# Kernel optimization log

Hardware: AMD Instinct MI355X
Metric: run time of the kernel (lower is better)

## Reference

```python
import jax, jax.numpy as jnp
import numpy as np
import math

DIM = 1024
THETA = 10000.0


def rope_cos_sin(seq_len, dim, dtype=jnp.float32):
    # freqs over pairs: 1/theta^(2i/dim), angles = t * freq
    inv = 1.0 / (THETA ** (jnp.arange(0, dim, 2, dtype=jnp.float32) / dim))  # [dim/2]
    t = jnp.arange(seq_len, dtype=jnp.float32)
    ang = jnp.outer(t, inv)  # [S, dim/2]
    return jnp.cos(ang).astype(dtype), jnp.sin(ang).astype(dtype)


def apply_rotary(x, cos, sin):
    # x: [B, S, D]; treat consecutive pairs as complex (xr + i*xi)
    B, S, D = x.shape
    xr = x[..., 0::2]  # [B, S, D/2]
    xi = x[..., 1::2]
    or_ = xr * cos - xi * sin
    oi_ = xr * sin + xi * cos
    # interleave back: (..., D/2, 2) -> (..., D)
    return jnp.stack([or_, oi_], axis=-1).reshape(B, S, D)


def setup_inputs() -> dict:
    key = jax.random.key(0)
    ks = jax.random.split(key, 5)
    B, S, D = 4, 2048, DIM
    x = jax.random.normal(ks[0], (B, S, D), dtype=jnp.float32)
    s = 1.0 / math.sqrt(D)
    wq = jax.random.normal(ks[1], (D, D), dtype=jnp.float32) * s
    wk = jax.random.normal(ks[2], (D, D), dtype=jnp.float32) * s
    wv = jax.random.normal(ks[3], (D, D), dtype=jnp.float32) * s
    wo = jax.random.normal(ks[4], (D, D), dtype=jnp.float32) * s
    return {"x": x, "wq": wq, "wk": wk, "wv": wv, "wo": wo}


def reference(x, wq, wk, wv, wo):
    B, S, D = x.shape
    xq = jnp.einsum('bsd,ed->bse', x, wq)  # Linear: x @ W^T
    xk = jnp.einsum('bsd,ed->bse', x, wk)
    xv = jnp.einsum('bsd,ed->bse', x, wv)
    cos, sin = rope_cos_sin(S, D, x.dtype)
    xq = apply_rotary(xq, cos, sin)
    xk = apply_rotary(xk, cos, sin)
    scores = jnp.einsum('bqd,bkd->bqk', xq, xk) / jnp.sqrt(jnp.asarray(D, x.dtype))
    attn = jax.nn.softmax(scores, axis=-1)  # no causal mask in original
    out = jnp.einsum('bqk,bkd->bqd', attn, xv)
    return jnp.einsum('bsd,ed->bse', out, wo)
```

## Files before the change

kernel.cpp:

```cpp
#include <hip/hip_runtime.h>
#include <math.h>

typedef __attribute__((ext_vector_type(8))) short short8;
typedef __attribute__((ext_vector_type(4))) float f32x4;
typedef unsigned short u16;

__device__ __forceinline__ float b2f(u16 u) {
    union { unsigned u; float f; } c; c.u = ((unsigned)u) << 16; return c.f;
}
__device__ __forceinline__ u16 f2b(float f) {
    unsigned u = __float_as_uint(f);
    u += 0x7fffu + ((u >> 16) & 1u);
    return (u16)(u >> 16);
}

__device__ __forceinline__ void gl_lds16(const u16* g, u16* l) {
    __builtin_amdgcn_global_load_lds(
        (const __attribute__((address_space(1))) void*)g,
        (__attribute__((address_space(3))) void*)l,
        16, 0, 0);
}

__global__ __launch_bounds__(256) void cvt_f32_bf16(const float* __restrict__ src,
                                                    u16* __restrict__ dst, int n) {
    const int i = (blockIdx.x * 256 + threadIdx.x) * 8;
    if (i >= n) return;
    const float4 a = *(const float4*)&src[i];
    const float4 b = *(const float4*)&src[i + 4];
    short8 o;
    o[0] = (short)f2b(a.x); o[1] = (short)f2b(a.y);
    o[2] = (short)f2b(a.z); o[3] = (short)f2b(a.w);
    o[4] = (short)f2b(b.x); o[5] = (short)f2b(b.y);
    o[6] = (short)f2b(b.z); o[7] = (short)f2b(b.w);
    *(short8*)&dst[i] = o;
}

__global__ __launch_bounds__(256) void cvt_weights(
    const float* __restrict__ w0, const float* __restrict__ w1,
    const float* __restrict__ w2, const float* __restrict__ w3,
    u16* __restrict__ dst) {
    const int z = blockIdx.z;
    const float* src = (z == 0) ? w0 : (z == 1) ? w1 : (z == 2) ? w2 : w3;
    const int i = (blockIdx.x * 256 + threadIdx.x) * 8;
    const float4 a = *(const float4*)&src[i];
    const float4 b = *(const float4*)&src[i + 4];
    short8 o;
    o[0] = (short)f2b(a.x); o[1] = (short)f2b(a.y);
    o[2] = (short)f2b(a.z); o[3] = (short)f2b(a.w);
    o[4] = (short)f2b(b.x); o[5] = (short)f2b(b.y);
    o[6] = (short)f2b(b.z); o[7] = (short)f2b(b.w);
    *(short8*)&dst[(long)z * 1024 * 1024 + i] = o;
}

template<typename OT>
__device__ __forceinline__ void gemm_body(
    const u16* __restrict__ A, const u16* __restrict__ W, OT* __restrict__ C,
    int lda, int ldw, int ldc, int K, float scale, int tm, int tn)
{
    __shared__ u16 lsA[2][128 * 32];
    __shared__ u16 lsB[2][128 * 32];

    const int m0 = tm * 128;
    const int n0 = tn * 128;
    const int t = threadIdx.x;
    const int lane = t & 63;
    const int wave = t >> 6;
    const int wm = (wave & 1) * 64;
    const int wn = (wave >> 1) * 64;

    const int sr = t >> 2;
    const int scol = ((t & 3) ^ ((t >> 3) & 3)) * 8;

    const int offA0 = (m0 + sr) * lda + scol;
    const int offA1 = offA0 + 64 * lda;
    const int offW0 = (n0 + sr) * ldw + scol;
    const int offW1 = offW0 + 64 * ldw;
    const u16* Au = A;
    const u16* Wu = W;

    f32x4 acc[4][4];
#pragma unroll
    for (int i = 0; i < 4; ++i)
#pragma unroll
        for (int j = 0; j < 4; ++j)
            acc[i][j] = (f32x4){0.f, 0.f, 0.f, 0.f};

    const int fr = lane & 15;
    const int fq = lane >> 4;
    const int swz = (fq ^ ((fr >> 1) & 3)) * 8;
    const int aoff = (wm + fr) * 32 + swz;
    const int boff = (wn + fr) * 32 + swz;

    auto prefetch = [&](int buf) {
        gl_lds16(Au + offA0, &lsA[buf][t * 8]);
        gl_lds16(Au + offA1, &lsA[buf][2048 + t * 8]);
        gl_lds16(Wu + offW0, &lsB[buf][t * 8]);
        gl_lds16(Wu + offW1, &lsB[buf][2048 + t * 8]);
        Au += 32;
        Wu += 32;
    };
    auto compute = [&](int buf) {
        short8 af[4], bf[4];
#pragma unroll
        for (int i = 0; i < 4; ++i)
            af[i] = *(const short8*)&lsA[buf][aoff + i * 512];
#pragma unroll
        for (int j = 0; j < 4; ++j)
            bf[j] = *(const short8*)&lsB[buf][boff + j * 512];
#pragma unroll
        for (int i = 0; i < 4; ++i)
#pragma unroll
            for (int j = 0; j < 4; ++j)
                acc[i][j] = __builtin_amdgcn_mfma_f32_16x16x32_bf16(af[i], bf[j], acc[i][j], 0, 0, 0);
    };

    const int nsteps = K >> 5;
    prefetch(0);
    for (int s = 0; s < nsteps; s += 2) {
        __syncthreads();
        prefetch(1);
        compute(0);
        __syncthreads();
        if (s + 2 < nsteps) prefetch(0);
        compute(1);
    }

#pragma unroll
    for (int i = 0; i < 4; ++i) {
#pragma unroll
        for (int j = 0; j < 4; ++j) {
            const int row0 = m0 + wm + i * 16 + fq * 4;
            const int col = n0 + wn + j * 16 + fr;
#pragma unroll
            for (int r = 0; r < 4; ++r) {
                const int row = row0 + r;
                const float val = acc[i][j][r] * scale;
                if (sizeof(OT) == 2) {
                    ((u16*)C)[(long)row * ldc + col] = f2b(val);
                } else {
                    ((float*)C)[(long)row * ldc + col] = val;
                }
            }
        }
    }
}

__global__ __launch_bounds__(256) void gemm_qkv(
    const u16* __restrict__ A, const u16* __restrict__ W, u16* __restrict__ C)
{
    const int id = blockIdx.x;
    const int xcd = id & 7;
    const int s = id >> 3;
    const int tn = s & 7;
    const int ml = (s >> 3) & 7;
    const int z = s >> 6;
    const int tm = xcd * 8 + ml;
    gemm_body<u16>(A, W + (long)z * (1024 * 1024), C + (long)z * (8 * 1024 * 1024),
                   1024, 1024, 1024, 1024, 1.0f, tm, tn);
}

__global__ __launch_bounds__(256) void gemm_dual(
    const u16* __restrict__ q, const u16* __restrict__ kk, u16* __restrict__ sc,
    const u16* __restrict__ wo, const u16* __restrict__ v, u16* __restrict__ UT)
{
    const long M1 = 1024 * 1024;
    const int id = blockIdx.x;
    const int xcd = id & 7;
    const int s = id >> 3;
    const int b = xcd >> 1;
    if (s < 128) {
        const int tn = s & 15;
        const int tm = (xcd & 1) * 8 + (s >> 4);
        gemm_body<u16>(q + b * 2 * M1, kk + b * 2 * M1, sc + b * 4 * M1,
                       1024, 1024, 2048, 1024, 0.03125f, tm, tn);
    } else if (s < 192) {
        const int s2 = s - 128;
        const int tn = s2 & 15;
        const int tm = (xcd & 1) * 4 + (s2 >> 4);
        gemm_body<u16>(wo, v + b * 2 * M1, UT + b * 2 * M1,
                       1024, 1024, 2048, 1024, 1.0f, tm, tn);
    }
}

__global__ __launch_bounds__(256) void gemm_pv(
    const u16* __restrict__ P, const u16* __restrict__ UT, float* __restrict__ out)
{
    const long M1 = 1024 * 1024;
    const int id = blockIdx.x;
    const int xcd = id & 7;
    const int s = id >> 3;
    const int b = xcd >> 1;
    const int tn = s & 7;
    const int tm = (xcd & 1) * 8 + (s >> 3);
    gemm_body<float>(P + b * 4 * M1, UT + b * 2 * M1, out + b * 2 * M1,
                     2048, 2048, 1024, 2048, 1.0f, tm, tn);
}

__global__ __launch_bounds__(256) void rope_kernel(u16* q, u16* k) {
    const int row = blockIdx.x;
    const int pos = row & 2047;
    u16* p = (blockIdx.y ? k : q) + (long)row * 1024;
#pragma unroll
    for (int it = 0; it < 2; ++it) {
        const int i = threadIdx.x + it * 256;
        const float e = (float)i * (1.0f / 512.0f);
        const float inv = powf(10000.0f, -e);
        const float ang = (float)pos * inv;
        float s, c;
        sincosf(ang, &s, &c);
        const float xr = b2f(p[2 * i]);
        const float xi = b2f(p[2 * i + 1]);
        p[2 * i]     = f2b(xr * c - xi * s);
        p[2 * i + 1] = f2b(xr * s + xi * c);
    }
}

__global__ __launch_bounds__(256) void softmax_kernel(const u16* __restrict__ S, u16* __restrict__ P) {
    const long row = blockIdx.x;
    const u16* src = S + row * 2048;
    u16* dst = P + row * 2048;
    const int t = threadIdx.x;
    const int lane = t & 63;
    const int wave = t >> 6;
    __shared__ float red[4];

    float v[8];
    const short8 raw = *(const short8*)&src[t * 8];
#pragma unroll
    for (int i = 0; i < 8; ++i) v[i] = b2f((u16)raw[i]);

    float m = v[0];
#pragma unroll
    for (int i = 1; i < 8; ++i) m = fmaxf(m, v[i]);
    for (int o = 32; o > 0; o >>= 1) m = fmaxf(m, __shfl_xor(m, o, 64));
    if (lane == 0) red[wave] = m;
    __syncthreads();
    m = fmaxf(fmaxf(red[0], red[1]), fmaxf(red[2], red[3]));
    __syncthreads();

    float sum = 0.f;
#pragma unroll
    for (int i = 0; i < 8; ++i) { v[i] = expf(v[i] - m); sum += v[i]; }
    for (int o = 32; o > 0; o >>= 1) sum += __shfl_xor(sum, o, 64);
    if (lane == 0) red[wave] = sum;
    __syncthreads();
    sum = red[0] + red[1] + red[2] + red[3];
    const float is = 1.0f / sum;

    short8 outv;
#pragma unroll
    for (int i = 0; i < 8; ++i) outv[i] = (short)f2b(v[i] * is);
    *(short8*)&dst[t * 8] = outv;
}

extern "C" void kernel_launch(void* const* d_in, const int* in_sizes, int n_in,
                              void* d_out, int out_size, void* d_ws, size_t ws_size,
                              hipStream_t stream)
{
    (void)in_sizes; (void)n_in; (void)out_size; (void)ws_size;
    const float* x  = (const float*)d_in[0];
    const float* wq = (const float*)d_in[1];
    const float* wk = (const float*)d_in[2];
    const float* wv = (const float*)d_in[3];
    const float* wo = (const float*)d_in[4];
    float* out = (float*)d_out;

    const long M1 = 1024 * 1024;
    u16* ws  = (u16*)d_ws;
    u16* xb  = ws;
    u16* wqb = xb + 8 * M1;
    u16* wob = wqb + 3 * M1;
    u16* q   = wqb + 4 * M1;
    u16* kk  = q + 8 * M1;
    u16* v   = kk + 8 * M1;
    u16* sc  = v + 8 * M1;
    u16* UT  = xb;

    const dim3 blk(256);

    cvt_f32_bf16<<<dim3(4096), blk, 0, stream>>>(x, xb, 8 * 1024 * 1024);
    cvt_weights<<<dim3(512, 1, 4), blk, 0, stream>>>(wq, wk, wv, wo, wqb);

    gemm_qkv<<<dim3(1536), blk, 0, stream>>>(xb, wqb, q);

    rope_kernel<<<dim3(8192, 2), blk, 0, stream>>>(q, kk);

    gemm_dual<<<dim3(2048), blk, 0, stream>>>(q, kk, sc, wob, v, UT);

    softmax_kernel<<<dim3(8192), blk, 0, stream>>>(sc, sc);

    gemm_pv<<<dim3(512), blk, 0, stream>>>(sc, UT, out);
}
```

Measured before the change: 328.5 us.

## Load GEMM fragments directly from global memory into registers, bypassing LDS

Removes the LDS double-buffer staging (global_load_lds plus barriers) in the shared GEMM body. Each wave now loads its own MFMA A/B fragments straight from global memory into a two-deep register buffer. This drops the __syncthreads and LDS traffic, but the tile is no longer shared across waves, so each A and B row is fetched by two waves. That doubles global/L2 load traffic and gives less coalesced 16-byte-per-lane accesses spread across strided rows.

After: 613.8 us. +86.9%, slower.

```diff
diff --git a/kernel.cpp b/kernel.cpp
--- a/kernel.cpp
+++ b/kernel.cpp
@@ -12,13 +12,6 @@
     unsigned u = __float_as_uint(f);
     u += 0x7fffu + ((u >> 16) & 1u);
     return (u16)(u >> 16);
-}
-
-__device__ __forceinline__ void gl_lds16(const u16* g, u16* l) {
-    __builtin_amdgcn_global_load_lds(
-        (const __attribute__((address_space(1))) void*)g,
-        (__attribute__((address_space(3))) void*)l,
-        16, 0, 0);
 }
 
 __global__ __launch_bounds__(256) void cvt_f32_bf16(const float* __restrict__ src,
@@ -57,9 +50,6 @@
     const u16* __restrict__ A, const u16* __restrict__ W, OT* __restrict__ C,
     int lda, int ldw, int ldc, int K, float scale, int tm, int tn)
 {
-    __shared__ u16 lsA[2][128 * 32];
-    __shared__ u16 lsB[2][128 * 32];
-
     const int m0 = tm * 128;
     const int n0 = tn * 128;
     const int t = threadIdx.x;
@@ -67,14 +57,14 @@
     const int wave = t >> 6;
     const int wm = (wave & 1) * 64;
     const int wn = (wave >> 1) * 64;
-
-    const int sr = t >> 2;
-    const int scol = ((t & 3) ^ ((t >> 3) & 3)) * 8;
-
-    const int offA0 = (m0 + sr) * lda + scol;
-    const int offA1 = offA0 + 64 * lda;
-    const int offW0 = (n0 + sr) * ldw + scol;
-    const int offW1 = offW0 + 64 * ldw;
+    const int fr = lane & 15;
+    const int fq = lane >> 4;
+
+    int offA[4], offB[4];
+#pragma unroll
+    for (int i = 0; i < 4; ++i) offA[i] = (m0 + wm + i * 16 + fr) * lda + fq * 8;
+#pragma unroll
+    for (int j = 0; j < 4; ++j) offB[j] = (n0 + wn + j * 16 + fr) * ldw + fq * 8;
     const u16* Au = A;
     const u16* Wu = W;
 
@@ -85,44 +75,41 @@
         for (int j = 0; j < 4; ++j)
             acc[i][j] = (f32x4){0.f, 0.f, 0.f, 0.f};
 
-    const int fr = lane & 15;
-    const int fq = lane >> 4;
-    const int swz = (fq ^ ((fr >> 1) & 3)) * 8;
-    const int aoff = (wm + fr) * 32 + swz;
-    const int boff = (wn + fr) * 32 + swz;
-
-    auto prefetch = [&](int buf) {
-        gl_lds16(Au + offA0, &lsA[buf][t * 8]);
-        gl_lds16(Au + offA1, &lsA[buf][2048 + t * 8]);
-        gl_lds16(Wu + offW0, &lsB[buf][t * 8]);
-        gl_lds16(Wu + offW1, &lsB[buf][2048 + t * 8]);
-        Au += 32;
-        Wu += 32;
-    };
-    auto compute = [&](int buf) {
-        short8 af[4], bf[4];
+    short8 af[2][4], bf[2][4];
+
+#pragma unroll
+    for (int i = 0; i < 4; ++i) af[0][i] = *(const short8*)(Au + offA[i]);
+#pragma unroll
+    for (int j = 0; j < 4; ++j) bf[0][j] = *(const short8*)(Wu + offB[j]);
+    Au += 32; Wu += 32;
+
+    const int nsteps = K >> 5;
+    for (int s = 0; s < nsteps; s += 2) {
+#pragma unroll
+        for (int i = 0; i < 4; ++i) af[1][i] = *(const short8*)(Au + offA[i]);
+#pragma unroll
+        for (int j = 0; j < 4; ++j) bf[1][j] = *(const short8*)(Wu + offB[j]);
+        Au += 32; Wu += 32;
+
 #pragma unroll
         for (int i = 0; i < 4; ++i)
-            af[i] = *(const short8*)&lsA[buf][aoff + i * 512];
-#pragma unroll
-        for (int j = 0; j < 4; ++j)
-            bf[j] = *(const short8*)&lsB[buf][boff + j * 512];
+#pragma unroll
+            for (int j = 0; j < 4; ++j)
+                acc[i][j] = __builtin_amdgcn_mfma_f32_16x16x32_bf16(af[0][i], bf[0][j], acc[i][j], 0, 0, 0);
+
+        if (s + 2 < nsteps) {
+#pragma unroll
+            for (int i = 0; i < 4; ++i) af[0][i] = *(const short8*)(Au + offA[i]);
+#pragma unroll
+            for (int j = 0; j < 4; ++j) bf[0][j] = *(const short8*)(Wu + offB[j]);
+            Au += 32; Wu += 32;
+        }
+
 #pragma unroll
         for (int i = 0; i < 4; ++i)
 #pragma unroll
             for (int j = 0; j < 4; ++j)
-                acc[i][j] = __builtin_amdgcn_mfma_f32_16x16x32_bf16(af[i], bf[j], acc[i][j], 0, 0, 0);
-    };
-
-    const int nsteps = K >> 5;
-    prefetch(0);
-    for (int s = 0; s < nsteps; s += 2) {
-        __syncthreads();
-        prefetch(1);
-        compute(0);
-        __syncthreads();
-        if (s + 2 < nsteps) prefetch(0);
-        compute(1);
+                acc[i][j] = __builtin_amdgcn_mfma_f32_16x16x32_bf16(af[1][i], bf[1][j], acc[i][j], 0, 0, 0);
     }
 
 #pragma unroll
```
